# Performance work log

Hardware: AMD Instinct MI355X
Metric: run time of the kernel (lower is better)

The kernel has to match this reference:

```python
import jax, jax.numpy as jnp
import numpy as np

# Config
SEQ_LEN = 512
PRED_LEN = 96
C = 64
TOPM = 4
N_WIRES = 6
PERIODS = [2, 3, 4]          # periods dividing pred_len (model.period_num)
N_SAMPLES = 5000             # size of retrieval table along sample axis
B = 128

# ---- tiny quantum circuit simulation helpers ----
# State vector over n_wires qubits: shape [bsz, 2**n_wires].

def apply_single_qubit_gate(state, gate, wire, n_wires):
    # state: [bsz, 2**n]; gate: [2,2]
    st = state.reshape((state.shape[0],) + (2,) * n_wires)
    axis = 1 + wire
    st = jnp.moveaxis(st, axis, -1)
    st = jnp.einsum('...i,ji->...j', st, gate)
    st = jnp.moveaxis(st, -1, axis)
    return st.reshape(state.shape)

def ry_gate(theta):
    c = jnp.cos(theta / 2.0)
    s = jnp.sin(theta / 2.0)
    return jnp.stack([jnp.stack([c, -s]), jnp.stack([s, c])])

def apply_ry_batched(state, thetas, wire, n_wires):
    # thetas: [bsz] -> per-sample gate
    c = jnp.cos(thetas / 2.0)
    s = jnp.sin(thetas / 2.0)
    st = state.reshape((state.shape[0],) + (2,) * n_wires)
    axis = 1 + wire
    st = jnp.moveaxis(st, axis, -1)
    a0 = st[..., 0]
    a1 = st[..., 1]
    shp = (thetas.shape[0],) + (1,) * (st.ndim - 2)
    cb = c.reshape(shp)
    sb = s.reshape(shp)
    n0 = cb * a0 - sb * a1
    n1 = sb * a0 + cb * a1
    st = jnp.stack([n0, n1], axis=-1)
    st = jnp.moveaxis(st, -1, axis)
    return st.reshape(state.shape)

def quantum_circuit(x_query, ansatz_angles, ansatz_wires):
    # x_query: [bsz, n_wires] encoder RY angles.
    bsz = x_query.shape[0]
    dim = 2 ** N_WIRES
    state = jnp.zeros((bsz, dim), dtype=x_query.dtype).at[:, 0].set(1.0)
    # encoder: RY(x_i) on wire i
    for w in range(N_WIRES):
        state = apply_ry_batched(state, x_query[:, w], w, N_WIRES)
    # ansatz: fixed random RY rotations (RandomLayer approximated by RY ops)
    for k in range(ansatz_angles.shape[0]):
        g = ry_gate(ansatz_angles[k])
        state = apply_single_qubit_gate(state, g, int(ansatz_wires[k]), N_WIRES)
    # measure PauliZ expectation on each wire
    probs = jnp.abs(state) ** 2  # [bsz, 2**n]
    basis = jnp.arange(dim)
    exps = []
    for w in range(N_WIRES):
        bit = (basis >> (N_WIRES - 1 - w)) & 1
        z = 1.0 - 2.0 * bit.astype(probs.dtype)
        exps.append(probs @ z)
    return jnp.stack(exps, axis=-1)  # [bsz, n_wires]


def setup_inputs() -> dict:
    key = jax.random.key(0)
    ks = jax.random.split(key, 16)
    inp = {}
    inp['x_enc'] = jax.random.normal(ks[0], (B, SEQ_LEN, C), jnp.float32)
    inp['index'] = jax.random.randint(ks[1], (B,), 0, N_SAMPLES)
    # params
    s = 1.0 / np.sqrt(SEQ_LEN)
    inp['W_query'] = jax.random.uniform(ks[2], (N_WIRES, SEQ_LEN), jnp.float32, -s, s)
    inp['b_query'] = jnp.zeros((N_WIRES,), jnp.float32)
    inp['W_x'] = jax.random.uniform(ks[3], (PRED_LEN, SEQ_LEN), jnp.float32, -s, s)
    inp['b_x'] = jnp.zeros((PRED_LEN,), jnp.float32)
    sw = 1.0 / np.sqrt(N_WIRES)
    inp['W_prob'] = jax.random.uniform(ks[4], (TOPM, N_WIRES), jnp.float32, -sw, sw)
    inp['b_prob'] = jnp.zeros((TOPM,), jnp.float32)
    # retrieval_pred linears: Linear(pred_len//g, pred_len)
    for i, g in enumerate(PERIODS):
        d = PRED_LEN // g
        sg = 1.0 / np.sqrt(d)
        inp[f'W_ret{i}'] = jax.random.uniform(jax.random.fold_in(ks[5], i), (PRED_LEN, d), jnp.float32, -sg, sg)
        inp[f'b_ret{i}'] = jnp.zeros((PRED_LEN,), jnp.float32)
    sc = 1.0 / np.sqrt(2 * PRED_LEN)
    inp['W_pred'] = jax.random.uniform(ks[6], (PRED_LEN, 2 * PRED_LEN), jnp.float32, -sc, sc)
    inp['b_pred'] = jnp.zeros((PRED_LEN,), jnp.float32)
    # retrieval table: [n_period, n_samples, topm, pred_len, C]
    inp['retrieval_table'] = jax.random.normal(ks[7], (len(PERIODS), N_SAMPLES, TOPM, PRED_LEN, C), jnp.float32) * 0.1
    # fixed ansatz (random layer) angles and wires
    n_ops = N_WIRES * 3
    inp['ansatz_angles'] = jax.random.uniform(ks[8], (n_ops,), jnp.float32, 0.0, 2 * np.pi)
    inp['ansatz_wires'] = jax.random.randint(ks[9], (n_ops,), 0, N_WIRES)
    # gumbel noise (pre-sampled for determinism)
    u = jax.random.uniform(ks[10], (B * C, TOPM), jnp.float32, 1e-6, 1.0 - 1e-6)
    inp['gumbel_noise'] = -jnp.log(-jnp.log(u))
    return inp


def reference(x_enc, index, W_query, b_query, W_x, b_x, W_prob, b_prob,
              W_ret0, b_ret0, W_ret1, b_ret1, W_ret2, b_ret2,
              W_pred, b_pred, retrieval_table, ansatz_angles, ansatz_wires,
              gumbel_noise):
    Bsz = x_enc.shape[0]
    x_offset = x_enc[:, -1:, :]                 # [B,1,C]
    x_norm = x_enc - x_offset                   # [B,S,C]
    xT = jnp.transpose(x_norm, (0, 2, 1))       # [B,C,S]
    base_pred = jnp.transpose(xT @ W_x.T + b_x, (0, 2, 1))  # [B,P,C]
    q_in = (xT @ W_query.T + b_query).reshape(Bsz * C, N_WIRES)
    exp_val = quantum_circuit(q_in, ansatz_angles, ansatz_wires)  # [B*C, n_wires]
    logits = exp_val @ W_prob.T + b_prob        # [B*C, topm]
    # gumbel-softmax hard, tau=0.5
    y_soft = jax.nn.softmax((logits + gumbel_noise) / 0.5, axis=-1)
    idx = jnp.argmax(y_soft, axis=-1)
    y_hard = jax.nn.one_hot(idx, TOPM, dtype=y_soft.dtype)
    weights = y_hard + y_soft - jax.lax.stop_gradient(y_soft)
    weights = jnp.transpose(weights.reshape(Bsz, C, TOPM), (0, 2, 1))  # [B,topm,C]
    # retrieval: table[i, index] -> [B, topm, P, C]
    Wr = [W_ret0, W_ret1, W_ret2]
    br = [b_ret0, b_ret1, b_ret2]
    raw = jnp.zeros((Bsz, TOPM, PRED_LEN, C), x_enc.dtype)
    for i, g in enumerate(PERIODS):
        pr = retrieval_table[i][index]                         # [B,topm,P,C]
        pr = pr.reshape(Bsz * TOPM, PRED_LEN // g, g, C)[:, :, 0, :]  # [B*topm, P//g, C]
        prT = jnp.transpose(pr, (0, 2, 1))                     # [B*topm, C, P//g]
        pr = jnp.transpose(prT @ Wr[i].T + br[i], (0, 2, 1))   # [B*topm, P, C]
        raw = raw + pr.reshape(Bsz, TOPM, PRED_LEN, C)
    selected = (raw * weights[:, :, None, :]).sum(axis=1)       # [B,P,C]
    combined = jnp.concatenate([base_pred, selected], axis=1)   # [B,2P,C]
    cT = jnp.transpose(combined, (0, 2, 1))
    pred_norm = jnp.transpose(cT @ W_pred.T + b_pred, (0, 2, 1))
    return pred_norm + x_offset
```

## Files before the change

### kernel.cpp

```cpp
#include <hip/hip_runtime.h>

typedef short bf16x8 __attribute__((ext_vector_type(8)));
typedef float f32x4  __attribute__((ext_vector_type(4)));

#define WS_CONST 30720
#define WS_QBIAS 30816

__device__ __forceinline__ short f2bf(float f) {
    unsigned u = __float_as_uint(f);
    unsigned r = (u + 0x7FFFu + ((u >> 16) & 1u)) >> 16;
    return (short)r;
}

__global__ __launch_bounds__(256) void prep_kernel(
    const float* __restrict__ W_query, const float* __restrict__ b_query,
    const float* __restrict__ W_x,     const float* __restrict__ b_x,
    const float* __restrict__ W_ret0,  const float* __restrict__ b_ret0,
    const float* __restrict__ W_ret1,  const float* __restrict__ b_ret1,
    const float* __restrict__ W_ret2,  const float* __restrict__ b_ret2,
    const float* __restrict__ W_pred,  const float* __restrict__ b_pred,
    const float* __restrict__ angles,  const int* __restrict__ wires,
    float* __restrict__ ws)
{
    const int bid = blockIdx.x;
    const int t = threadIdx.x;
    __shared__ float wp[9216];
    __shared__ float wsl[768];
    short* ap = (short*)ws;

    if (bid < 80) {
        const bool isM1 = bid < 64;
        for (int L = t; L < 9216; L += 256) {
            int r = L / 96, k = L - r * 96;
            wp[L] = W_pred[r * 192 + (isM1 ? k : 96 + k)];
        }
        if (isM1) {
            const int s0 = bid * 8;
            for (int L = t; L < 768; L += 256) {
                int k = L >> 3, s = L & 7;
                wsl[L] = W_x[k * 512 + s0 + s];
            }
        } else {
            const int j0 = (bid - 64) * 8;
            for (int L = t; L < 768; L += 256) {
                int k = L >> 3, jj = L & 7;
                int j = j0 + jj;
                float v = 0.f;
                if (j < 104) {
                    const float* Wr; int d, jl;
                    if (j < 48)      { Wr = W_ret0; d = 48; jl = j; }
                    else if (j < 80) { Wr = W_ret1; d = 32; jl = j - 48; }
                    else             { Wr = W_ret2; d = 24; jl = j - 80; }
                    v = Wr[k * d + jl];
                }
                wsl[L] = v;
            }
        }
        __syncthreads();
        #pragma unroll
        for (int i = 0; i < 3; ++i) {
            int idx = t + i * 256;
            int r = idx >> 3, s = idx & 7;
            float acc = 0.f;
            #pragma unroll 8
            for (int k = 0; k < 96; ++k) acc += wp[r * 96 + k] * wsl[k * 8 + s];
            int sg = isM1 ? (bid * 8 + s) : (512 + (bid - 64) * 8 + s);
            int kstep = sg >> 5, s32 = sg & 31;
            int g = s32 >> 3, e = s32 & 7;
            ap[kstep * 3072 + (r >> 4) * 512 + (g * 16 + (r & 15)) * 8 + e] = f2bf(acc);
        }
    } else {
        if (t < 96) {
            float v = b_pred[t];
            for (int k = 0; k < 96; ++k) {
                v += W_pred[t * 192 + k] * b_x[k];
                v += W_pred[t * 192 + 96 + k] * (b_ret0[k] + b_ret1[k] + b_ret2[k]);
            }
            ws[WS_CONST + t] = v;
        } else if (t < 102) {
            int w = t - 96;
            float v = b_query[w];
            for (int k = 0; k < 18; ++k)
                if (wires[k] == w) v += angles[k];
            ws[WS_QBIAS + w] = v;
        }
    }
}

__global__ __launch_bounds__(512) void main_kernel(
    const float* __restrict__ x_enc,
    const int*   __restrict__ index,
    const float* __restrict__ W_query,
    const float* __restrict__ W_prob,
    const float* __restrict__ b_prob,
    const float* __restrict__ RT,
    const float* __restrict__ gumbel,
    const float* __restrict__ ws,
    float* __restrict__ out)
{
    const int bid = blockIdx.x;
    const int b = bid & 127;
    const int cbase = (bid >> 7) * 16;
    const int t = threadIdx.x;
    const int lane = t & 63;
    const int wv = t >> 6;

    __shared__ __align__(16) union {
        struct { float wq[3072]; float qp[3072]; } s0;
        char Abuf[24576];
    } u0;
    __shared__ __align__(16) short xbuf[16][520];
    __shared__ __align__(16) union {
        float qfin[96];
        short selbuf[16][136];
    } u1;
    __shared__ int m_sel[16];

    const float* __restrict__ xb = x_enc + (size_t)b * 32768;

    {
        const float4* wsrc = (const float4*)W_query;
        float4* wdst = (float4*)u0.s0.wq;
        for (int L = t; L < 768; L += 512) wdst[L] = wsrc[L];
    }

    const int c  = t & 15;
    const int sg = t >> 4;
    const float xo = xb[511 * 64 + cbase + c];
    const float* xs = xb + (size_t)(sg * 16) * 64 + cbase + c;
    float v[16];
    #pragma unroll
    for (int i = 0; i < 16; ++i) v[i] = xs[i * 64];

    __syncthreads();

    {
        #pragma unroll
        for (int i = 0; i < 16; ++i) v[i] -= xo;
        const float4* wq4 = (const float4*)u0.s0.wq;
        float* qp = u0.s0.qp;
        #pragma unroll
        for (int wr = 0; wr < 6; ++wr) {
            float a = 0.f;
            #pragma unroll
            for (int i4 = 0; i4 < 4; ++i4) {
                float4 w4 = wq4[wr * 128 + sg * 4 + i4];
                a += w4.x * v[i4*4+0] + w4.y * v[i4*4+1] + w4.z * v[i4*4+2] + w4.w * v[i4*4+3];
            }
            qp[sg * 96 + wr * 16 + c] = a;
        }
        short* xrow = &xbuf[c][sg * 16];
        #pragma unroll
        for (int i = 0; i < 16; i += 2) {
            unsigned lo = (unsigned short)f2bf(v[i]);
            unsigned hi = (unsigned short)f2bf(v[i+1]);
            *(unsigned*)&xrow[i] = lo | (hi << 16);
        }
    }
    __syncthreads();

    if (t < 96) {
        int w6 = t >> 4, cc = t & 15;
        const float* qp = u0.s0.qp;
        float s = 0.f;
        #pragma unroll
        for (int g2 = 0; g2 < 32; ++g2) s += qp[g2 * 96 + w6 * 16 + cc];
        u1.qfin[w6 * 16 + cc] = s;
    }
    __syncthreads();

    if (t < 16) {
        float e[6];
        #pragma unroll
        for (int w = 0; w < 6; ++w) e[w] = cosf(u1.qfin[w * 16 + t] + ws[WS_QBIAS + w]);
        int grow = (b * 64 + cbase + t) * 4;
        float best = -1e30f; int bm = 0;
        #pragma unroll
        for (int m = 0; m < 4; ++m) {
            float lg = b_prob[m];
            #pragma unroll
            for (int w = 0; w < 6; ++w) lg += W_prob[m * 6 + w] * e[w];
            lg += gumbel[grow + m];
            if (lg > best) { best = lg; bm = m; }
        }
        m_sel[t] = bm;
    }
    __syncthreads();

    {
        const int idxb = index[b];
        for (int L = t; L < 16 * 136; L += 512) {
            int cc = L & 15, j = L >> 4;
            short val = 0;
            if (j < 104) {
                int i, row;
                if (j < 48)      { i = 0; row = j * 2; }
                else if (j < 80) { i = 1; row = (j - 48) * 3; }
                else             { i = 2; row = (j - 80) * 4; }
                val = f2bf(RT[(size_t)i * 122880000ull + (size_t)idxb * 24576ull
                             + (size_t)m_sel[cc] * 6144ull + (size_t)row * 64ull + cbase + cc]);
            }
            u1.selbuf[cc][j] = val;
        }
    }

    const char* Apack = (const char*)ws;
    const int cl = lane & 15, g = lane >> 4;
    f32x4 acc0 = {0,0,0,0};
    for (int ch = 0; ch < 5; ++ch) {
        const float4* asrc = (const float4*)(Apack + ch * 24576);
        float4 r0 = asrc[t], r1 = asrc[t + 512], r2 = asrc[t + 1024];
        __syncthreads();
        float4* adst = (float4*)u0.Abuf;
        adst[t] = r0; adst[t + 512] = r1; adst[t + 1024] = r2;
        __syncthreads();
        if (wv < 6) {
            #pragma unroll
            for (int ks = 0; ks < 4; ++ks) {
                bf16x8 av = *(const bf16x8*)(u0.Abuf + ks * 6144 + wv * 1024 + lane * 16);
                bf16x8 bv0;
                if (ch < 4) bv0 = *(const bf16x8*)&xbuf[cl][ch * 128 + ks * 32 + g * 8];
                else        bv0 = *(const bf16x8*)&u1.selbuf[cl][ks * 32 + g * 8];
                acc0 = __builtin_amdgcn_mfma_f32_16x16x32_bf16(av, bv0, acc0, 0, 0, 0);
            }
        }
    }

    if (wv < 6) {
        const float* cst = ws + WS_CONST;
        float xo0 = xb[511 * 64 + cbase + cl];
        int r0 = wv * 16 + g * 4;
        float* op = out + (size_t)b * 6144 + (size_t)r0 * 64 + cbase;
        #pragma unroll
        for (int reg = 0; reg < 4; ++reg)
            op[reg * 64 + cl] = acc0[reg] + cst[r0 + reg] + xo0;
    }
}

extern "C" void kernel_launch(void* const* d_in, const int* in_sizes, int n_in,
                              void* d_out, int out_size, void* d_ws, size_t ws_size,
                              hipStream_t stream) {
    (void)in_sizes; (void)n_in; (void)out_size; (void)ws_size;
    const float* x_enc   = (const float*)d_in[0];
    const int*   index   = (const int*)d_in[1];
    const float* W_query = (const float*)d_in[2];
    const float* b_query = (const float*)d_in[3];
    const float* W_x     = (const float*)d_in[4];
    const float* b_x     = (const float*)d_in[5];
    const float* W_prob  = (const float*)d_in[6];
    const float* b_prob  = (const float*)d_in[7];
    const float* W_ret0  = (const float*)d_in[8];
    const float* b_ret0  = (const float*)d_in[9];
    const float* W_ret1  = (const float*)d_in[10];
    const float* b_ret1  = (const float*)d_in[11];
    const float* W_ret2  = (const float*)d_in[12];
    const float* b_ret2  = (const float*)d_in[13];
    const float* W_pred  = (const float*)d_in[14];
    const float* b_pred  = (const float*)d_in[15];
    const float* RT      = (const float*)d_in[16];
    const float* angles  = (const float*)d_in[17];
    const int*   wires   = (const int*)d_in[18];
    const float* gumbel  = (const float*)d_in[19];
    float* out = (float*)d_out;
    float* ws  = (float*)d_ws;

    prep_kernel<<<81, 256, 0, stream>>>(W_query, b_query, W_x, b_x,
                                        W_ret0, b_ret0, W_ret1, b_ret1, W_ret2, b_ret2,
                                        W_pred, b_pred, angles, wires, ws);
    main_kernel<<<512, 512, 0, stream>>>(x_enc, index, W_query, W_prob, b_prob,
                                         RT, gumbel, ws, out);
}
```

Measured before the change: 24.69 us.

## Fuse weight-prep kernel into main kernel with chained per-block MFMA GEMMs

Removes the separate prep kernel that precomputed W_pred·[W_x; W_ret] as a packed bf16 matrix in workspace. Each block now does two stages: it multiplies W_x and the retrieval weights by its x and selected rows, writes the bf16 intermediates to shared memory, then applies W_pred with a third MFMA. Weights are loaded from global fp32 and converted to bf16 in registers, and the query bias is computed inline. This saves a kernel launch and the dependency between the two kernels, but every block repeats the weight conversion, adds an extra barrier, and introduces an extra bf16 rounding of the intermediate.

```diff
diff --git a/kernel.cpp b/kernel.cpp
--- a/kernel.cpp
+++ b/kernel.cpp
@@ -2,9 +2,6 @@
 
 typedef short bf16x8 __attribute__((ext_vector_type(8)));
 typedef float f32x4  __attribute__((ext_vector_type(4)));
-
-#define WS_CONST 30720
-#define WS_QBIAS 30816
 
 __device__ __forceinline__ short f2bf(float f) {
     unsigned u = __float_as_uint(f);
@@ -12,90 +9,22 @@
     return (short)r;
 }
 
-__global__ __launch_bounds__(256) void prep_kernel(
-    const float* __restrict__ W_query, const float* __restrict__ b_query,
-    const float* __restrict__ W_x,     const float* __restrict__ b_x,
+__global__ __launch_bounds__(512) void fused_kernel(
+    const float* __restrict__ x_enc,
+    const int*   __restrict__ index,
+    const float* __restrict__ W_query,
+    const float* __restrict__ b_query,
+    const float* __restrict__ W_x,
+    const float* __restrict__ b_x,
+    const float* __restrict__ W_prob,
+    const float* __restrict__ b_prob,
     const float* __restrict__ W_ret0,  const float* __restrict__ b_ret0,
     const float* __restrict__ W_ret1,  const float* __restrict__ b_ret1,
     const float* __restrict__ W_ret2,  const float* __restrict__ b_ret2,
     const float* __restrict__ W_pred,  const float* __restrict__ b_pred,
+    const float* __restrict__ RT,
     const float* __restrict__ angles,  const int* __restrict__ wires,
-    float* __restrict__ ws)
-{
-    const int bid = blockIdx.x;
-    const int t = threadIdx.x;
-    __shared__ float wp[9216];
-    __shared__ float wsl[768];
-    short* ap = (short*)ws;
-
-    if (bid < 80) {
-        const bool isM1 = bid < 64;
-        for (int L = t; L < 9216; L += 256) {
-            int r = L / 96, k = L - r * 96;
-            wp[L] = W_pred[r * 192 + (isM1 ? k : 96 + k)];
-        }
-        if (isM1) {
-            const int s0 = bid * 8;
-            for (int L = t; L < 768; L += 256) {
-                int k = L >> 3, s = L & 7;
-                wsl[L] = W_x[k * 512 + s0 + s];
-            }
-        } else {
-            const int j0 = (bid - 64) * 8;
-            for (int L = t; L < 768; L += 256) {
-                int k = L >> 3, jj = L & 7;
-                int j = j0 + jj;
-                float v = 0.f;
-                if (j < 104) {
-                    const float* Wr; int d, jl;
-                    if (j < 48)      { Wr = W_ret0; d = 48; jl = j; }
-                    else if (j < 80) { Wr = W_ret1; d = 32; jl = j - 48; }
-                    else             { Wr = W_ret2; d = 24; jl = j - 80; }
-                    v = Wr[k * d + jl];
-                }
-                wsl[L] = v;
-            }
-        }
-        __syncthreads();
-        #pragma unroll
-        for (int i = 0; i < 3; ++i) {
-            int idx = t + i * 256;
-            int r = idx >> 3, s = idx & 7;
-            float acc = 0.f;
-            #pragma unroll 8
-            for (int k = 0; k < 96; ++k) acc += wp[r * 96 + k] * wsl[k * 8 + s];
-            int sg = isM1 ? (bid * 8 + s) : (512 + (bid - 64) * 8 + s);
-            int kstep = sg >> 5, s32 = sg & 31;
-            int g = s32 >> 3, e = s32 & 7;
-            ap[kstep * 3072 + (r >> 4) * 512 + (g * 16 + (r & 15)) * 8 + e] = f2bf(acc);
-        }
-    } else {
-        if (t < 96) {
-            float v = b_pred[t];
-            for (int k = 0; k < 96; ++k) {
-                v += W_pred[t * 192 + k] * b_x[k];
-                v += W_pred[t * 192 + 96 + k] * (b_ret0[k] + b_ret1[k] + b_ret2[k]);
-            }
-            ws[WS_CONST + t] = v;
-        } else if (t < 102) {
-            int w = t - 96;
-            float v = b_query[w];
-            for (int k = 0; k < 18; ++k)
-                if (wires[k] == w) v += angles[k];
-            ws[WS_QBIAS + w] = v;
-        }
-    }
-}
-
-__global__ __launch_bounds__(512) void main_kernel(
-    const float* __restrict__ x_enc,
-    const int*   __restrict__ index,
-    const float* __restrict__ W_query,
-    const float* __restrict__ W_prob,
-    const float* __restrict__ b_prob,
-    const float* __restrict__ RT,
     const float* __restrict__ gumbel,
-    const float* __restrict__ ws,
     float* __restrict__ out)
 {
     const int bid = blockIdx.x;
@@ -104,10 +33,11 @@
     const int t = threadIdx.x;
     const int lane = t & 63;
     const int wv = t >> 6;
+    const int cl = lane & 15, g = lane >> 4;
 
     __shared__ __align__(16) union {
         struct { float wq[3072]; float qp[3072]; } s0;
-        char Abuf[24576];
+        short tbuf[16][200];
     } u0;
     __shared__ __align__(16) short xbuf[16][520];
     __shared__ __align__(16) union {
@@ -170,9 +100,16 @@
     __syncthreads();
 
     if (t < 16) {
+        float qb[6];
+        #pragma unroll
+        for (int w = 0; w < 6; ++w) {
+            float s = b_query[w];
+            for (int k2 = 0; k2 < 18; ++k2) s += (wires[k2] == w) ? angles[k2] : 0.f;
+            qb[w] = s;
+        }
         float e[6];
         #pragma unroll
-        for (int w = 0; w < 6; ++w) e[w] = cosf(u1.qfin[w * 16 + t] + ws[WS_QBIAS + w]);
+        for (int w = 0; w < 6; ++w) e[w] = cosf(u1.qfin[w * 16 + t] + qb[w]);
         int grow = (b * 64 + cbase + t) * 4;
         float best = -1e30f; int bm = 0;
         #pragma unroll
@@ -203,44 +140,91 @@
             u1.selbuf[cc][j] = val;
         }
     }
-
-    const char* Apack = (const char*)ws;
-    const int cl = lane & 15, g = lane >> 4;
-    f32x4 acc0 = {0,0,0,0};
-    for (int ch = 0; ch < 5; ++ch) {
-        const float4* asrc = (const float4*)(Apack + ch * 24576);
-        float4 r0 = asrc[t], r1 = asrc[t + 512], r2 = asrc[t + 1024];
-        __syncthreads();
-        float4* adst = (float4*)u0.Abuf;
-        adst[t] = r0; adst[t + 512] = r1; adst[t + 1024] = r2;
-        __syncthreads();
-        if (wv < 6) {
-            #pragma unroll
-            for (int ks = 0; ks < 4; ++ks) {
-                bf16x8 av = *(const bf16x8*)(u0.Abuf + ks * 6144 + wv * 1024 + lane * 16);
-                bf16x8 bv0;
-                if (ch < 4) bv0 = *(const bf16x8*)&xbuf[cl][ch * 128 + ks * 32 + g * 8];
-                else        bv0 = *(const bf16x8*)&u1.selbuf[cl][ks * 32 + g * 8];
-                acc0 = __builtin_amdgcn_mfma_f32_16x16x32_bf16(av, bv0, acc0, 0, 0, 0);
+    __syncthreads();
+
+    if (wv < 6) {
+        const int arow = wv * 16 + cl;
+        const int r0 = wv * 16 + g * 4;
+
+        f32x4 acc1 = {0,0,0,0};
+        const float* wxr = W_x + (size_t)arow * 512 + g * 8;
+        #pragma unroll 4
+        for (int ks = 0; ks < 16; ++ks) {
+            float4 w0 = *(const float4*)(wxr + ks * 32);
+            float4 w1 = *(const float4*)(wxr + ks * 32 + 4);
+            bf16x8 av;
+            av[0]=f2bf(w0.x); av[1]=f2bf(w0.y); av[2]=f2bf(w0.z); av[3]=f2bf(w0.w);
+            av[4]=f2bf(w1.x); av[5]=f2bf(w1.y); av[6]=f2bf(w1.z); av[7]=f2bf(w1.w);
+            bf16x8 bv = *(const bf16x8*)&xbuf[cl][ks * 32 + g * 8];
+            acc1 = __builtin_amdgcn_mfma_f32_16x16x32_bf16(av, bv, acc1, 0, 0, 0);
+        }
+        {
+            unsigned p0, p1;
+            float bx0 = b_x[r0], bx1 = b_x[r0+1], bx2 = b_x[r0+2], bx3 = b_x[r0+3];
+            p0 = (unsigned short)f2bf(acc1[0] + bx0) | ((unsigned)(unsigned short)f2bf(acc1[1] + bx1) << 16);
+            p1 = (unsigned short)f2bf(acc1[2] + bx2) | ((unsigned)(unsigned short)f2bf(acc1[3] + bx3) << 16);
+            unsigned* dst = (unsigned*)&u0.tbuf[cl][r0];
+            dst[0] = p0; dst[1] = p1;
+        }
+
+        f32x4 acc2 = {0,0,0,0};
+        #pragma unroll
+        for (int ks = 0; ks < 4; ++ks) {
+            int kk = ks * 32 + g * 8;
+            bf16x8 av = {0,0,0,0,0,0,0,0};
+            if (kk < 104) {
+                const float* p;
+                if (kk < 48)      p = W_ret0 + (size_t)arow * 48 + kk;
+                else if (kk < 80) p = W_ret1 + (size_t)arow * 32 + (kk - 48);
+                else              p = W_ret2 + (size_t)arow * 24 + (kk - 80);
+                float4 w0 = *(const float4*)p;
+                float4 w1 = *(const float4*)(p + 4);
+                av[0]=f2bf(w0.x); av[1]=f2bf(w0.y); av[2]=f2bf(w0.z); av[3]=f2bf(w0.w);
+                av[4]=f2bf(w1.x); av[5]=f2bf(w1.y); av[6]=f2bf(w1.z); av[7]=f2bf(w1.w);
             }
-        }
-    }
+            bf16x8 bv = *(const bf16x8*)&u1.selbuf[cl][ks * 32 + g * 8];
+            acc2 = __builtin_amdgcn_mfma_f32_16x16x32_bf16(av, bv, acc2, 0, 0, 0);
+        }
+        {
+            float bs0 = b_ret0[r0]   + b_ret1[r0]   + b_ret2[r0];
+            float bs1 = b_ret0[r0+1] + b_ret1[r0+1] + b_ret2[r0+1];
+            float bs2 = b_ret0[r0+2] + b_ret1[r0+2] + b_ret2[r0+2];
+            float bs3 = b_ret0[r0+3] + b_ret1[r0+3] + b_ret2[r0+3];
+            unsigned p0 = (unsigned short)f2bf(acc2[0] + bs0) | ((unsigned)(unsigned short)f2bf(acc2[1] + bs1) << 16);
+            unsigned p1 = (unsigned short)f2bf(acc2[2] + bs2) | ((unsigned)(unsigned short)f2bf(acc2[3] + bs3) << 16);
+            unsigned* dst = (unsigned*)&u0.tbuf[cl][96 + r0];
+            dst[0] = p0; dst[1] = p1;
+        }
+    }
+    __syncthreads();
 
     if (wv < 6) {
-        const float* cst = ws + WS_CONST;
+        const int arow = wv * 16 + cl;
+        const int r0 = wv * 16 + g * 4;
+        f32x4 acc3 = {0,0,0,0};
+        const float* wpr = W_pred + (size_t)arow * 192 + g * 8;
+        #pragma unroll
+        for (int ks = 0; ks < 6; ++ks) {
+            float4 w0 = *(const float4*)(wpr + ks * 32);
+            float4 w1 = *(const float4*)(wpr + ks * 32 + 4);
+            bf16x8 av;
+            av[0]=f2bf(w0.x); av[1]=f2bf(w0.y); av[2]=f2bf(w0.z); av[3]=f2bf(w0.w);
+            av[4]=f2bf(w1.x); av[5]=f2bf(w1.y); av[6]=f2bf(w1.z); av[7]=f2bf(w1.w);
+            bf16x8 bv = *(const bf16x8*)&u0.tbuf[cl][ks * 32 + g * 8];
+            acc3 = __builtin_amdgcn_mfma_f32_16x16x32_bf16(av, bv, acc3, 0, 0, 0);
+        }
         float xo0 = xb[511 * 64 + cbase + cl];
-        int r0 = wv * 16 + g * 4;
         float* op = out + (size_t)b * 6144 + (size_t)r0 * 64 + cbase;
         #pragma unroll
         for (int reg = 0; reg < 4; ++reg)
-            op[reg * 64 + cl] = acc0[reg] + cst[r0 + reg] + xo0;
+            op[reg * 64 + cl] = acc3[reg] + b_pred[r0 + reg] + xo0;
     }
 }
 
 extern "C" void kernel_launch(void* const* d_in, const int* in_sizes, int n_in,
                               void* d_out, int out_size, void* d_ws, size_t ws_size,
                               hipStream_t stream) {
-    (void)in_sizes; (void)n_in; (void)out_size; (void)ws_size;
+    (void)in_sizes; (void)n_in; (void)out_size; (void)d_ws; (void)ws_size;
     const float* x_enc   = (const float*)d_in[0];
     const int*   index   = (const int*)d_in[1];
     const float* W_query = (const float*)d_in[2];
@@ -262,11 +246,9 @@
     const int*   wires   = (const int*)d_in[18];
     const float* gumbel  = (const float*)d_in[19];
     float* out = (float*)d_out;
-    float* ws  = (float*)d_ws;
-
-    prep_kernel<<<81, 256, 0, stream>>>(W_query, b_query, W_x, b_x,
-                                        W_ret0, b_ret0, W_ret1, b_ret1, W_ret2, b_ret2,
-                                        W_pred, b_pred, angles, wires, ws);
-    main_kernel<<<512, 512, 0, stream>>>(x_enc, index, W_query, W_prob, b_prob,
-                                         RT, gumbel, ws, out);
+
+    fused_kernel<<<512, 512, 0, stream>>>(x_enc, index, W_query, b_query, W_x, b_x,
+                                          W_prob, b_prob,
+                                          W_ret0, b_ret0, W_ret1, b_ret1, W_ret2, b_ret2,
+                                          W_pred, b_pred, RT, angles, wires, gumbel, out);
 }
```

Result: slower. 32.32 us (+30.9%).

## Warp-specialize: overlap retrieval gather with MFMA, load A directly from global

Applied to the files above, without the earlier changes.

Replaces the five-chunk LDS staging of the packed weight matrix (each chunk guarded by two barriers) with per-lane direct global loads of the A fragments. The two spare waves gather the retrieval table rows while the six compute waves run the x-part MFMAs concurrently. A single barrier then precedes the selected-part MFMAs. This removes about ten block barriers and the LDS copy, but relies on cache hits for the A loads, which are now repeated per block without a shared staging buffer.

```diff
diff --git a/kernel.cpp b/kernel.cpp
--- a/kernel.cpp
+++ b/kernel.cpp
@@ -104,11 +104,9 @@
     const int t = threadIdx.x;
     const int lane = t & 63;
     const int wv = t >> 6;
-
-    __shared__ __align__(16) union {
-        struct { float wq[3072]; float qp[3072]; } s0;
-        char Abuf[24576];
-    } u0;
+    const int cl = lane & 15, g = lane >> 4;
+
+    __shared__ __align__(16) struct { float wq[3072]; float qp[3072]; } s0;
     __shared__ __align__(16) short xbuf[16][520];
     __shared__ __align__(16) union {
         float qfin[96];
@@ -120,7 +118,7 @@
 
     {
         const float4* wsrc = (const float4*)W_query;
-        float4* wdst = (float4*)u0.s0.wq;
+        float4* wdst = (float4*)s0.wq;
         for (int L = t; L < 768; L += 512) wdst[L] = wsrc[L];
     }
 
@@ -137,8 +135,8 @@
     {
         #pragma unroll
         for (int i = 0; i < 16; ++i) v[i] -= xo;
-        const float4* wq4 = (const float4*)u0.s0.wq;
-        float* qp = u0.s0.qp;
+        const float4* wq4 = (const float4*)s0.wq;
+        float* qp = s0.qp;
         #pragma unroll
         for (int wr = 0; wr < 6; ++wr) {
             float a = 0.f;
@@ -161,7 +159,7 @@
 
     if (t < 96) {
         int w6 = t >> 4, cc = t & 15;
-        const float* qp = u0.s0.qp;
+        const float* qp = s0.qp;
         float s = 0.f;
         #pragma unroll
         for (int g2 = 0; g2 < 32; ++g2) s += qp[g2 * 96 + w6 * 16 + cc];
@@ -187,9 +185,13 @@
     }
     __syncthreads();
 
-    {
+    const char* Ap = (const char*)ws;
+    const char* arow_base = Ap + wv * 1024 + lane * 16;
+    f32x4 acc = {0,0,0,0};
+    if (wv >= 6) {
+        const int t2 = t - 384;
         const int idxb = index[b];
-        for (int L = t; L < 16 * 136; L += 512) {
+        for (int L = t2; L < 16 * 136; L += 128) {
             int cc = L & 15, j = L >> 4;
             short val = 0;
             if (j < 104) {
@@ -202,38 +204,30 @@
             }
             u1.selbuf[cc][j] = val;
         }
-    }
-
-    const char* Apack = (const char*)ws;
-    const int cl = lane & 15, g = lane >> 4;
-    f32x4 acc0 = {0,0,0,0};
-    for (int ch = 0; ch < 5; ++ch) {
-        const float4* asrc = (const float4*)(Apack + ch * 24576);
-        float4 r0 = asrc[t], r1 = asrc[t + 512], r2 = asrc[t + 1024];
-        __syncthreads();
-        float4* adst = (float4*)u0.Abuf;
-        adst[t] = r0; adst[t + 512] = r1; adst[t + 1024] = r2;
-        __syncthreads();
-        if (wv < 6) {
-            #pragma unroll
-            for (int ks = 0; ks < 4; ++ks) {
-                bf16x8 av = *(const bf16x8*)(u0.Abuf + ks * 6144 + wv * 1024 + lane * 16);
-                bf16x8 bv0;
-                if (ch < 4) bv0 = *(const bf16x8*)&xbuf[cl][ch * 128 + ks * 32 + g * 8];
-                else        bv0 = *(const bf16x8*)&u1.selbuf[cl][ks * 32 + g * 8];
-                acc0 = __builtin_amdgcn_mfma_f32_16x16x32_bf16(av, bv0, acc0, 0, 0, 0);
-            }
-        }
-    }
+    } else {
+        #pragma unroll 4
+        for (int ks = 0; ks < 16; ++ks) {
+            bf16x8 av = *(const bf16x8*)(arow_base + ks * 6144);
+            bf16x8 bv = *(const bf16x8*)&xbuf[cl][ks * 32 + g * 8];
+            acc = __builtin_amdgcn_mfma_f32_16x16x32_bf16(av, bv, acc, 0, 0, 0);
+        }
+    }
+    __syncthreads();
 
     if (wv < 6) {
+        #pragma unroll
+        for (int ks = 0; ks < 4; ++ks) {
+            bf16x8 av = *(const bf16x8*)(arow_base + (16 + ks) * 6144);
+            bf16x8 bv = *(const bf16x8*)&u1.selbuf[cl][ks * 32 + g * 8];
+            acc = __builtin_amdgcn_mfma_f32_16x16x32_bf16(av, bv, acc, 0, 0, 0);
+        }
         const float* cst = ws + WS_CONST;
         float xo0 = xb[511 * 64 + cbase + cl];
         int r0 = wv * 16 + g * 4;
         float* op = out + (size_t)b * 6144 + (size_t)r0 * 64 + cbase;
         #pragma unroll
         for (int reg = 0; reg < 4; ++reg)
-            op[reg * 64 + cl] = acc0[reg] + cst[r0 + reg] + xo0;
+            op[reg * 64 + cl] = acc[reg] + cst[r0 + reg] + xo0;
     }
 }
 
```

Result: slower. 26.04 us (+5.5%).

## Fuse weight-prep kernel into main kernel with global atomic counter handoff

Applied to the files above, without the earlier changes.

Removes the separate prep kernel and has the first 121 blocks of the main grid compute the packed W_pred·W_x / W_pred·W_ret product matrix and the constant bias before doing their own work. Each of those blocks signals completion through an agent-scope atomic counter. All blocks spin on that counter just before the MFMA stage, so the prep work overlaps with their x loading, query and gather phases. The per-wire query bias is now computed inline per block. This saves one kernel launch and its serialization gap, but adds a memset, a spin-wait that relies on all 512 blocks being co-resident or the prep blocks being scheduled first, and redundant bias work in every block.

```diff
diff --git a/kernel.cpp b/kernel.cpp
--- a/kernel.cpp
+++ b/kernel.cpp
@@ -4,7 +4,7 @@
 typedef float f32x4  __attribute__((ext_vector_type(4)));
 
 #define WS_CONST 30720
-#define WS_QBIAS 30816
+#define WS_CTR   30816
 
 __device__ __forceinline__ short f2bf(float f) {
     unsigned u = __float_as_uint(f);
@@ -12,90 +12,23 @@
     return (short)r;
 }
 
-__global__ __launch_bounds__(256) void prep_kernel(
-    const float* __restrict__ W_query, const float* __restrict__ b_query,
-    const float* __restrict__ W_x,     const float* __restrict__ b_x,
+__global__ __launch_bounds__(512) void fused_kernel(
+    const float* __restrict__ x_enc,
+    const int*   __restrict__ index,
+    const float* __restrict__ W_query,
+    const float* __restrict__ b_query,
+    const float* __restrict__ W_x,
+    const float* __restrict__ b_x,
+    const float* __restrict__ W_prob,
+    const float* __restrict__ b_prob,
     const float* __restrict__ W_ret0,  const float* __restrict__ b_ret0,
     const float* __restrict__ W_ret1,  const float* __restrict__ b_ret1,
     const float* __restrict__ W_ret2,  const float* __restrict__ b_ret2,
     const float* __restrict__ W_pred,  const float* __restrict__ b_pred,
+    const float* __restrict__ RT,
     const float* __restrict__ angles,  const int* __restrict__ wires,
-    float* __restrict__ ws)
-{
-    const int bid = blockIdx.x;
-    const int t = threadIdx.x;
-    __shared__ float wp[9216];
-    __shared__ float wsl[768];
-    short* ap = (short*)ws;
-
-    if (bid < 80) {
-        const bool isM1 = bid < 64;
-        for (int L = t; L < 9216; L += 256) {
-            int r = L / 96, k = L - r * 96;
-            wp[L] = W_pred[r * 192 + (isM1 ? k : 96 + k)];
-        }
-        if (isM1) {
-            const int s0 = bid * 8;
-            for (int L = t; L < 768; L += 256) {
-                int k = L >> 3, s = L & 7;
-                wsl[L] = W_x[k * 512 + s0 + s];
-            }
-        } else {
-            const int j0 = (bid - 64) * 8;
-            for (int L = t; L < 768; L += 256) {
-                int k = L >> 3, jj = L & 7;
-                int j = j0 + jj;
-                float v = 0.f;
-                if (j < 104) {
-                    const float* Wr; int d, jl;
-                    if (j < 48)      { Wr = W_ret0; d = 48; jl = j; }
-                    else if (j < 80) { Wr = W_ret1; d = 32; jl = j - 48; }
-                    else             { Wr = W_ret2; d = 24; jl = j - 80; }
-                    v = Wr[k * d + jl];
-                }
-                wsl[L] = v;
-            }
-        }
-        __syncthreads();
-        #pragma unroll
-        for (int i = 0; i < 3; ++i) {
-            int idx = t + i * 256;
-            int r = idx >> 3, s = idx & 7;
-            float acc = 0.f;
-            #pragma unroll 8
-            for (int k = 0; k < 96; ++k) acc += wp[r * 96 + k] * wsl[k * 8 + s];
-            int sg = isM1 ? (bid * 8 + s) : (512 + (bid - 64) * 8 + s);
-            int kstep = sg >> 5, s32 = sg & 31;
-            int g = s32 >> 3, e = s32 & 7;
-            ap[kstep * 3072 + (r >> 4) * 512 + (g * 16 + (r & 15)) * 8 + e] = f2bf(acc);
-        }
-    } else {
-        if (t < 96) {
-            float v = b_pred[t];
-            for (int k = 0; k < 96; ++k) {
-                v += W_pred[t * 192 + k] * b_x[k];
-                v += W_pred[t * 192 + 96 + k] * (b_ret0[k] + b_ret1[k] + b_ret2[k]);
-            }
-            ws[WS_CONST + t] = v;
-        } else if (t < 102) {
-            int w = t - 96;
-            float v = b_query[w];
-            for (int k = 0; k < 18; ++k)
-                if (wires[k] == w) v += angles[k];
-            ws[WS_QBIAS + w] = v;
-        }
-    }
-}
-
-__global__ __launch_bounds__(512) void main_kernel(
-    const float* __restrict__ x_enc,
-    const int*   __restrict__ index,
-    const float* __restrict__ W_query,
-    const float* __restrict__ W_prob,
-    const float* __restrict__ b_prob,
-    const float* __restrict__ RT,
     const float* __restrict__ gumbel,
-    const float* __restrict__ ws,
+    float* __restrict__ ws,
     float* __restrict__ out)
 {
     const int bid = blockIdx.x;
@@ -104,6 +37,7 @@
     const int t = threadIdx.x;
     const int lane = t & 63;
     const int wv = t >> 6;
+    const int cl = lane & 15, g = lane >> 4;
 
     __shared__ __align__(16) union {
         struct { float wq[3072]; float qp[3072]; } s0;
@@ -116,6 +50,48 @@
     } u1;
     __shared__ int m_sel[16];
 
+    unsigned* ctr = (unsigned*)(ws + WS_CTR);
+    short* ap = (short*)ws;
+
+    if (bid < 120) {
+        const int rr = (bid / 20) * 16 + (t >> 5);
+        const int kk = (bid % 20) * 32 + (t & 31);
+        float a = 0.f;
+        if (kk < 512) {
+            const float* pr = W_pred + rr * 192;
+            #pragma unroll 8
+            for (int q = 0; q < 96; ++q) a += pr[q] * W_x[q * 512 + kk];
+        } else {
+            const int j = kk - 512;
+            if (j < 104) {
+                const float* Wr; int d, jl;
+                if (j < 48)      { Wr = W_ret0; d = 48; jl = j; }
+                else if (j < 80) { Wr = W_ret1; d = 32; jl = j - 48; }
+                else             { Wr = W_ret2; d = 24; jl = j - 80; }
+                const float* pr = W_pred + rr * 192 + 96;
+                #pragma unroll 8
+                for (int q = 0; q < 96; ++q) a += pr[q] * Wr[q * d + jl];
+            }
+        }
+        ap[(kk >> 5) * 3072 + (rr >> 4) * 512
+           + (((kk & 31) >> 3) * 16 + (rr & 15)) * 8 + (kk & 7)] = f2bf(a);
+    } else if (bid == 120) {
+        if (t < 96) {
+            float vv = b_pred[t];
+            const float* pr = W_pred + t * 192;
+            for (int q = 0; q < 96; ++q)
+                vv += pr[q] * b_x[q] + pr[96 + q] * (b_ret0[q] + b_ret1[q] + b_ret2[q]);
+            ws[WS_CONST + t] = vv;
+        }
+    }
+    if (bid <= 120) {
+        __syncthreads();
+        if (t == 0) {
+            __threadfence();
+            __hip_atomic_fetch_add(ctr, 1u, __ATOMIC_RELEASE, __HIP_MEMORY_SCOPE_AGENT);
+        }
+    }
+
     const float* __restrict__ xb = x_enc + (size_t)b * 32768;
 
     {
@@ -170,9 +146,16 @@
     __syncthreads();
 
     if (t < 16) {
+        float qb[6];
+        #pragma unroll
+        for (int w = 0; w < 6; ++w) {
+            float s = b_query[w];
+            for (int k2 = 0; k2 < 18; ++k2) s += (wires[k2] == w) ? angles[k2] : 0.f;
+            qb[w] = s;
+        }
         float e[6];
         #pragma unroll
-        for (int w = 0; w < 6; ++w) e[w] = cosf(u1.qfin[w * 16 + t] + ws[WS_QBIAS + w]);
+        for (int w = 0; w < 6; ++w) e[w] = cosf(u1.qfin[w * 16 + t] + qb[w]);
         int grow = (b * 64 + cbase + t) * 4;
         float best = -1e30f; int bm = 0;
         #pragma unroll
@@ -204,13 +187,19 @@
         }
     }
 
+    if (t == 0) {
+        while (__hip_atomic_load(ctr, __ATOMIC_RELAXED, __HIP_MEMORY_SCOPE_AGENT) < 121u)
+            __builtin_amdgcn_s_sleep(4);
+        (void)__hip_atomic_load(ctr, __ATOMIC_ACQUIRE, __HIP_MEMORY_SCOPE_AGENT);
+    }
+    __syncthreads();
+
     const char* Apack = (const char*)ws;
-    const int cl = lane & 15, g = lane >> 4;
     f32x4 acc0 = {0,0,0,0};
     for (int ch = 0; ch < 5; ++ch) {
         const float4* asrc = (const float4*)(Apack + ch * 24576);
         float4 r0 = asrc[t], r1 = asrc[t + 512], r2 = asrc[t + 1024];
-        __syncthreads();
+        if (ch) __syncthreads();
         float4* adst = (float4*)u0.Abuf;
         adst[t] = r0; adst[t + 512] = r1; adst[t + 1024] = r2;
         __syncthreads();
@@ -264,9 +253,10 @@
     float* out = (float*)d_out;
     float* ws  = (float*)d_ws;
 
-    prep_kernel<<<81, 256, 0, stream>>>(W_query, b_query, W_x, b_x,
-                                        W_ret0, b_ret0, W_ret1, b_ret1, W_ret2, b_ret2,
-                                        W_pred, b_pred, angles, wires, ws);
-    main_kernel<<<512, 512, 0, stream>>>(x_enc, index, W_query, W_prob, b_prob,
-                                         RT, gumbel, ws, out);
+    hipMemsetAsync((char*)ws + WS_CTR * 4, 0, 4, stream);
+    fused_kernel<<<512, 512, 0, stream>>>(x_enc, index, W_query, b_query, W_x, b_x,
+                                          W_prob, b_prob,
+                                          W_ret0, b_ret0, W_ret1, b_ret1, W_ret2, b_ret2,
+                                          W_pred, b_pred, RT, angles, wires, gumbel,
+                                          ws, out);
 }
```

Measured after the change: 36.04 us. 46.0% more time.
